# Kernel tuning notes

Hardware: AMD Instinct MI355X
Metric: run time of the kernel (lower is better)

Reference implementation:

```python
import jax, jax.numpy as jnp
import numpy as np

N, M, K, R, D = 2048, 64, 2, 512, 1024   # seq len, chunk size, neighbours, neighbour len, model dim
H, L = 16, 1024                           # heads, layer_size
LCH = N // M                              # number of chunks l = 32
DH = L // H
SCALE = 1.0 / (D ** 0.5)                  # source scales by input dim, not head dim


def setup_inputs() -> dict:
    key = jax.random.key(0)
    ks = jax.random.split(key, 6)
    s = 0.02
    return {
        "x": jax.random.normal(ks[0], (N, D), jnp.float32),
        "neighbours": jax.random.normal(ks[1], (LCH, K, R, D), jnp.float32),
        "Wq": jax.random.normal(ks[2], (L, D), jnp.float32) * s,
        "Wk": jax.random.normal(ks[3], (L, D), jnp.float32) * s,
        "Wv": jax.random.normal(ks[4], (L, D), jnp.float32) * s,
        "Wo": jax.random.normal(ks[5], (D, L), jnp.float32) * s,
    }


def _attend(q_in, ctx, Wq, Wk, Wv, Wo):
    # q_in: (B, Q, D) queries; ctx: (B, K, R, D) retrieved neighbours.
    # Batches the per-chunk, per-neighbour Attention calls of the source in one pass,
    # then means over the K neighbour axis (reduce 'k m d -> m d', 'mean').
    B, Q = q_in.shape[0], q_in.shape[1]
    q = (q_in @ Wq.T).reshape(B, Q, H, DH)                     # (B,Q,H,DH)
    kk = (ctx @ Wk.T).reshape(B, K, R, H, DH)                  # (B,K,R,H,DH)
    vv = (ctx @ Wv.T).reshape(B, K, R, H, DH)
    scores = jnp.einsum('bqhe,bkrhe->bkhrq', q, kk) * SCALE    # (B,K,H,R,Q)
    # FAITHFUL quirk: source softmaxes over the QUERY axis (last dim of 'b k q')
    w = jax.nn.softmax(scores, axis=-1)
    o = jnp.einsum('bkhrq,bkrhe->bkqhe', w, vv).reshape(B, K, Q, L)
    z = jnp.einsum('bkql,dl->bkqd', o, Wo)                     # output projection (dropout=0)
    return z.mean(axis=1)                                      # mean over neighbours -> (B,Q,D)


def reference(x, neighbours, Wq, Wk, Wv, Wo):
    # attending_chunks: shift input left by m-1, zero-pad bottom, chunk into (l, m, d)
    att = jnp.concatenate([x[M - 1:], jnp.zeros((M - 1, D), x.dtype)], axis=0).reshape(LCH, M, D)
    # main loop over chunks u in [0, l-2] and their k neighbours, fully batched
    main = _attend(att[:LCH - 1], neighbours[:LCH - 1], Wq, Wk, Wv, Wo)   # (l-1, M, D)
    # last token attends to neighbours[-1]
    last = _attend(x[-1][None, None, :], neighbours[-1][None], Wq, Wk, Wv, Wo)  # (1,1,D)
    body = jnp.concatenate([main.reshape(-1, D), att[-1]], axis=0)        # (N, D)
    # pad top with m-1 zeros, keep first n rows
    out = jnp.concatenate([jnp.zeros((M - 1, D), x.dtype), body[:N - M + 1]], axis=0)
    out = out.at[:M - 1].set(x[:M - 1])
    out = out.at[-1].set(last[0, 0])
    return out
```

## Files before the change

kernel.cpp:

```cpp
#include <hip/hip_runtime.h>
#include <hip/hip_bf16.h>


using u16 = unsigned short;
using u32 = unsigned int;

typedef float  f32x4   __attribute__((ext_vector_type(4)));
typedef __bf16 bf16x8v __attribute__((ext_vector_type(8)));
typedef __bf16 bf16x4v __attribute__((ext_vector_type(4)));
typedef short  s16x4   __attribute__((ext_vector_type(4)));
typedef u16    u16x8   __attribute__((ext_vector_type(8)));
typedef u16    u16x4v  __attribute__((ext_vector_type(4)));

#define SCALE_LOG2E (1.4426950408889634f / 32.0f)

__device__ __forceinline__ u16 f2b(float f){ return __builtin_bit_cast(u16, (__bf16)f); }
__device__ __forceinline__ int swz(int row, int cb){ return row*128 + (cb ^ ((row & 7) << 4)); }

__device__ __forceinline__ void gl_lds16(const void* g, void* l) {
    __builtin_amdgcn_global_load_lds(
        (const __attribute__((address_space(1))) unsigned int*)(unsigned long long)g,
        (__attribute__((address_space(3))) unsigned int*)(unsigned int)(unsigned long long)l,
        16, 0, 0);
}

__global__ __launch_bounds__(512, 2)
void gemm256(const u16* __restrict__ Ap, const u16* __restrict__ Bp,
             u16* __restrict__ Ka, u16* __restrict__ Vt,
             const u16* __restrict__ Aq, const u16* __restrict__ Bq,
             u16* __restrict__ Qa,
             int nKV, int nNt)
{
    __shared__ char Ls[131072];
    char* const Abase = Ls;
    char* const Bbase = Ls + 65536;

    const int tid  = threadIdx.x;
    const int lane = tid & 63, wave = tid >> 6;
    const int li = lane & 15, lg = lane >> 4;
    const int wr = wave >> 2, wc = wave & 3;

    const int nwg  = gridDim.x;
    const int lin  = blockIdx.x;
    const int lin2 = (lin & 7) * (nwg >> 3) + (lin >> 3);

    const bool isQ = (lin2 >= nKV);
    long bm, bn;
    if (isQ) { const int idx = lin2 - nKV; bm = (long)(idx >> 2) * 256; bn = (long)(idx & 3) * 256; }
    else     {                              bm = (long)(lin2 / nNt) * 256; bn = (long)(lin2 % nNt) * 256; }
    const u16* const Ag = isQ ? Aq : Ap;
    const u16* const Bg = isQ ? Bq : Bp;

    const int srow = tid >> 3;
    const int scol = ((tid & 7) ^ (srow & 7)) << 3;

    const u16* const pA0 = Ag + (bm + srow)*1024L + scol;
    const u16* const pA1 = Ag + (bm + 128 + srow)*1024L + scol;
    const u16* const pB0 = Bg + (bn + srow)*1024L + scol;
    const u16* const pB1 = Bg + (bn + 128 + srow)*1024L + scol;
    const long l64 = 64*1024L;

    auto stA = [&](int t, int hh) {
        char* d = Abase + (t & 1)*32768 + hh*16384 + wave*1024;
        const u16* p = (hh ? pA1 : pA0) + (long)t*64;
        gl_lds16(p, d);
        gl_lds16(p + l64, d + 8192);
    };
    auto stB = [&](int t, int hh) {
        char* d = Bbase + (t & 1)*32768 + hh*16384 + wave*1024;
        const u16* p = (hh ? pB1 : pB0) + (long)t*64;
        gl_lds16(p, d);
        gl_lds16(p + l64, d + 8192);
    };

    const int NT = 16;

    stB(0, 0); stB(0, 1); stA(0, 0); stA(0, 1); stB(1, 0);
    asm volatile("s_waitcnt vmcnt(2)" ::: "memory");
    asm volatile("s_barrier" ::: "memory");

    const int swx = (li & 7) << 4;
    const int cb0 = (lg*16) ^ swx;
    const int cb1 = (64 + lg*16) ^ swx;
    const int brb = (wc & 1)*64 + li;

    f32x4 acc[8][4] = {};
    bf16x8v av[4], aw[4], bv[4];

#define MFMA16(MH, AA, BB)                                                      \
    __builtin_amdgcn_s_setprio(1);                                              \
    _Pragma("unroll") for (int mt = 0; mt < 4; mt++)                            \
        _Pragma("unroll") for (int nt = 0; nt < 4; nt++)                        \
            acc[(MH)*4 + mt][nt] = __builtin_amdgcn_mfma_f32_16x16x32_bf16(     \
                (AA)[mt], (BB)[nt], acc[(MH)*4 + mt][nt], 0, 0, 0);             \
    __builtin_amdgcn_s_setprio(0);
#define RDA(DST, OFS, CB)                                                       \
    _Pragma("unroll") for (int i = 0; i < 4; i++)                               \
        (DST)[i] = *(const bf16x8v*)(At + (li + (OFS) + i*16)*128 + (CB));
#define RDB(DST, CB)                                                            \
    _Pragma("unroll") for (int i = 0; i < 4; i++)                               \
        (DST)[i] = *(const bf16x8v*)(Bt + (brb + i*16)*128 + (CB));

    for (int t = 0; t < NT; ++t) {
        char* At = Abase + (t & 1)*32768 + wr*16384;
        char* Bt = Bbase + (t & 1)*32768 + (wc >> 1)*16384;
        const bool s1 = (t + 1 < NT), s2 = (t + 2 < NT);

        RDA(av, 0, cb0); RDB(bv, cb0);
        if (s1) { stB(t + 1, 1); stA(t + 1, 0); }
        RDA(aw, 64, cb0);
        __builtin_amdgcn_sched_barrier(0);
        MFMA16(0, av, bv);
        if (s1) stA(t + 1, 1);
        RDA(av, 0, cb1);
        __builtin_amdgcn_sched_barrier(0);
        MFMA16(1, aw, bv);
        RDB(bv, cb1); RDA(aw, 64, cb1);
        __builtin_amdgcn_sched_barrier(0);
        MFMA16(0, av, bv);
        asm volatile("s_barrier" ::: "memory");
        if (s2) stB(t + 2, 0);
        MFMA16(1, aw, bv);
        if      (s2) { asm volatile("s_waitcnt vmcnt(2)" ::: "memory"); }
        else if (s1) { asm volatile("s_waitcnt vmcnt(0)" ::: "memory"); }
        asm volatile("s_barrier" ::: "memory");
    }
#undef MFMA16
#undef RDA
#undef RDB

    if (!isQ && bn >= 1024) {
        #pragma unroll
        for (int ai = 0; ai < 8; ai++) {
            const int m0 = wr*128 + (ai >> 2)*64 + (ai & 3)*16 + lg*4;
            #pragma unroll
            for (int nt = 0; nt < 4; nt++) {
                const int n = wc*64 + nt*16 + li;
                f32x4 c = acc[ai][nt];
                bf16x4v w;
                #pragma unroll
                for (int j = 0; j < 4; j++) w[j] = (__bf16)c[j];
                *(bf16x4v*)(Ls + n*512 + ((m0*2) ^ ((n & 31) << 4))) = w;
            }
        }
        __syncthreads();
        const int n    = tid >> 1;
        const int half = (tid & 1) * 128;
        u16* dst = Vt + (bn - 1024 + n)*32768L + bm + half;
        #pragma unroll
        for (int i = 0; i < 16; i++) {
            const int mb = (half + i*8) * 2;
            uint4 v = *(const uint4*)(Ls + n*512 + (mb ^ ((n & 31) << 4)));
            *(uint4*)(dst + i*8) = v;
        }
    } else {
        u16* Co = isQ ? Qa : Ka;
        #pragma unroll
        for (int ai = 0; ai < 8; ai++) {
            #pragma unroll
            for (int nt = 0; nt < 4; nt++) {
                f32x4 c = acc[ai][nt];
                const long row0 = bm + wr*128 + (ai >> 2)*64 + (ai & 3)*16 + lg*4;
                const long col  = bn + wc*64 + nt*16 + li;
                #pragma unroll
                for (int j = 0; j < 4; j++)
                    Co[(row0 + j)*1024 + col] = f2b(c[j]);
            }
        }
    }
}

template<bool AF32, int OM>
__global__ __launch_bounds__(256)
void gemm128(const void* __restrict__ Ap, int lda,
             const u16* __restrict__ Bp, int ldb,
             void* __restrict__ Cp, void* __restrict__ Cp2,
             int M, int Kc, int row_off, int nNt)
{
    __shared__ char As[128*128];
    __shared__ char Bs[128*128];
    const int tid  = threadIdx.x;
    const int lane = tid & 63, wave = tid >> 6;
    const int li = lane & 15, lg = lane >> 4;
    const int wr = wave >> 1, wc = wave & 1;

    const int nwg  = gridDim.x;
    const int lin  = blockIdx.x;
    const int lin2 = (lin & 7) * (nwg >> 3) + (lin >> 3);
    const long bm = (long)(lin2 / nNt) * 128;
    const long bn = (long)(lin2 % nNt) * 128;

    const int grow = wave*32 + (lane >> 3);
    const int gcol = ((lane & 7) ^ (lane >> 3)) << 3;
    const int sr = tid >> 1, sc = (tid & 1) * 32;
    long arow_f = bm + sr; if (arow_f >= M) arow_f = M - 1;
    long arow_g[4];
    #pragma unroll
    for (int j = 0; j < 4; j++) {
        long r = bm + grow + j*8;
        arow_g[j] = (r < M) ? r : (M - 1);
    }

    f32x4 acc[4][4] = {};

    for (int k0 = 0; k0 < Kc; k0 += 64) {
        float4 a4[8];
        if (AF32) {
            const float4* ap = (const float4*)((const float*)Ap + arow_f*lda + k0 + sc);
            #pragma unroll
            for (int i = 0; i < 8; i++) a4[i] = ap[i];
        }
        __syncthreads();
        if (!AF32) {
            #pragma unroll
            for (int j = 0; j < 4; j++)
                gl_lds16((const u16*)Ap + arow_g[j]*(long)lda + k0 + gcol,
                         As + (wave*4 + j)*1024);
        }
        #pragma unroll
        for (int j = 0; j < 4; j++)
            gl_lds16(Bp + (bn + grow + j*8)*(long)ldb + k0 + gcol,
                     Bs + (wave*4 + j)*1024);
        if (AF32) {
            #pragma unroll
            for (int i = 0; i < 4; i++) {
                float4 f0 = a4[2*i], f1 = a4[2*i+1];
                bf16x8v w;
                w[0]=(__bf16)f0.x; w[1]=(__bf16)f0.y; w[2]=(__bf16)f0.z; w[3]=(__bf16)f0.w;
                w[4]=(__bf16)f1.x; w[5]=(__bf16)f1.y; w[6]=(__bf16)f1.z; w[7]=(__bf16)f1.w;
                *(bf16x8v*)(As + swz(sr, sc*2 + i*16)) = w;
            }
        }
        __syncthreads();
        #pragma unroll
        for (int es = 0; es < 2; es++) {
            bf16x8v af[4], bfv[4];
            #pragma unroll
            for (int mt = 0; mt < 4; mt++)
                af[mt] = *(const bf16x8v*)(As + swz(wr*64 + mt*16 + li, es*64 + lg*16));
            #pragma unroll
            for (int nt = 0; nt < 4; nt++)
                bfv[nt] = *(const bf16x8v*)(Bs + swz(wc*64 + nt*16 + li, es*64 + lg*16));
            #pragma unroll
            for (int mt = 0; mt < 4; mt++)
                #pragma unroll
                for (int nt = 0; nt < 4; nt++)
                    acc[mt][nt] = __builtin_amdgcn_mfma_f32_16x16x32_bf16(
                        af[mt], bfv[nt], acc[mt][nt], 0, 0, 0);
        }
    }

    #pragma unroll
    for (int mt = 0; mt < 4; mt++) {
        #pragma unroll
        for (int nt = 0; nt < 4; nt++) {
            f32x4 c = acc[mt][nt];
            const long row0 = bm + wr*64 + mt*16 + lg*4;
            const long col  = bn + wc*64 + nt*16 + li;
            if (OM == 0) {
                u16* C = (u16*)Cp;
                #pragma unroll
                for (int j = 0; j < 4; j++) {
                    long rg = row0 + j;
                    if (rg < M) C[rg*1024 + col] = f2b(c[j]);
                }
            } else if (OM == 2) {
                float* C = (float*)Cp;
                #pragma unroll
                for (int j = 0; j < 4; j++) {
                    long rg = row0 + j;
                    if (rg < M) C[(row_off + rg)*1024 + col] = c[j];
                }
            } else {
                if (col < 1024) {
                    u16* Ka = (u16*)Cp;
                    #pragma unroll
                    for (int j = 0; j < 4; j++) Ka[(row0 + j)*1024 + col] = f2b(c[j]);
                } else {
                    u16* Vt = (u16*)Cp2;
                    bf16x4v w;
                    #pragma unroll
                    for (int j = 0; j < 4; j++) w[j] = (__bf16)c[j];
                    *(bf16x4v*)(Vt + (col - 1024)*32768L + row0) = w;
                }
            }
        }
    }
}

__global__ __launch_bounds__(256)
void attn_kernel(const u16* __restrict__ Qa, const u16* __restrict__ Ka,
                 const u16* __restrict__ Vt, u16* __restrict__ Om,
                 const float* __restrict__ x, float* __restrict__ out)
{
    const int u = blockIdx.x, h = blockIdx.y;
    const int tid = threadIdx.x;
    const int lane = tid & 63, wave = tid >> 6;
    const int li = lane & 15, lg = lane >> 4;

    if (u == 31) {
        #pragma unroll 4
        for (int it = 0; it < 16; ++it) {
            const int row = h*64 + it*4 + wave;
            const u16* p = Vt + (long)row*32768 + 31*1024 + lane*16;
            float s = 0.f;
            #pragma unroll
            for (int hf = 0; hf < 2; hf++) {
                bf16x8v v = *(const bf16x8v*)(p + hf*8);
                #pragma unroll
                for (int i = 0; i < 8; i++) s += (float)v[i];
            }
            #pragma unroll
            for (int m = 1; m < 64; m <<= 1) s += __shfl_xor(s, m);
            if (lane == 0) Om[(long)1984*1024 + row] = f2b(0.5f * s);
        }
        for (int i = h*1008 + tid; i < (h + 1)*1008; i += 256)
            ((float4*)out)[i] = ((const float4*)x)[i];
        return;
    }

    bf16x8v qf[4][2];
    #pragma unroll
    for (int qt = 0; qt < 4; qt++)
        #pragma unroll
        for (int es = 0; es < 2; es++)
            qf[qt][es] = *(const bf16x8v*)(Qa + (long)(63 + u*64 + qt*16 + li)*1024
                                              + h*64 + es*32 + lg*8);

    f32x4 acc[4][4] = {};

    for (int it = wave; it < 64; it += 4) {
        const int k = it >> 5, rsub = it & 31;
        const long kr = (long)u*1024 + k*512 + rsub*16;

        bf16x8v a0 = *(const bf16x8v*)(Ka + (kr + li)*1024 + h*64 + lg*8);
        bf16x8v a1 = *(const bf16x8v*)(Ka + (kr + li)*1024 + h*64 + 32 + lg*8);
        s16x4 va[4];
        #pragma unroll
        for (int et = 0; et < 4; et++)
            va[et] = *(const s16x4*)(Vt + (long)(h*64 + et*16 + li)*32768 + kr + lg*4);

        f32x4 s[4];
        #pragma unroll
        for (int qt = 0; qt < 4; qt++) {
            f32x4 c = {};
            c = __builtin_amdgcn_mfma_f32_16x16x32_bf16(a0, qf[qt][0], c, 0, 0, 0);
            c = __builtin_amdgcn_mfma_f32_16x16x32_bf16(a1, qf[qt][1], c, 0, 0, 0);
            s[qt] = c;
        }
        float p[4][4];
        #pragma unroll
        for (int qt = 0; qt < 4; qt++)
            #pragma unroll
            for (int j = 0; j < 4; j++)
                p[qt][j] = __builtin_amdgcn_exp2f(s[qt][j]);
        float rz[4];
        #pragma unroll
        for (int j = 0; j < 4; j++) {
            float z = p[0][j] + p[1][j] + p[2][j] + p[3][j];
            z += __shfl_xor(z, 1); z += __shfl_xor(z, 2);
            z += __shfl_xor(z, 4); z += __shfl_xor(z, 8);
            rz[j] = __builtin_amdgcn_rcpf(z);
        }
        s16x4 wf[4];
        #pragma unroll
        for (int qt = 0; qt < 4; qt++) {
            bf16x4v w;
            #pragma unroll
            for (int j = 0; j < 4; j++) w[j] = (__bf16)(p[qt][j] * rz[j]);
            wf[qt] = __builtin_bit_cast(s16x4, w);
        }
        #pragma unroll
        for (int et = 0; et < 4; et++)
            #pragma unroll
            for (int qt = 0; qt < 4; qt++)
                acc[et][qt] = __builtin_amdgcn_mfma_f32_16x16x16bf16_1k(
                    va[et], wf[qt], acc[et][qt], 0, 0, 0);
    }

    __shared__ float Osum[64*64];
    for (int w = 0; w < 4; w++) {
        if (wave == w) {
            #pragma unroll
            for (int et = 0; et < 4; et++)
                #pragma unroll
                for (int qt = 0; qt < 4; qt++)
                    #pragma unroll
                    for (int j = 0; j < 4; j++) {
                        int e = et*16 + lg*4 + j, q = qt*16 + li;
                        if (w == 0) Osum[e*64 + q]  = acc[et][qt][j];
                        else        Osum[e*64 + q] += acc[et][qt][j];
                    }
        }
        __syncthreads();
    }
    const int q = tid & 63, e0 = (tid >> 6) * 16;
    u16x8 o0, o1;
    #pragma unroll
    for (int i = 0; i < 8; i++) {
        o0[i] = f2b(0.5f * Osum[(e0 + i    )*64 + q]);
        o1[i] = f2b(0.5f * Osum[(e0 + 8 + i)*64 + q]);
    }
    u16* dst = Om + (long)(u*64 + q)*1024 + h*64 + e0;
    *(u16x8*)dst       = o0;
    *(u16x8*)(dst + 8) = o1;
}

__global__ __launch_bounds__(256)
void convert_all(const float* __restrict__ Wq, const float* __restrict__ Wk,
                 const float* __restrict__ Wv, const float* __restrict__ Wo,
                 const float* __restrict__ nb, const float* __restrict__ x,
                 u16* __restrict__ wW, u16* __restrict__ Anb,
                 u16* __restrict__ xb, int doA)
{
    const int NW = 524288, NN = 4194304, NX = 262144;
    const int tot = doA ? (NW + NN + NX) : NW;
    const int stride = gridDim.x*256;
    for (int i = blockIdx.x*256 + threadIdx.x; i < tot; i += stride) {
        const float* s; u16* d; float sc = 1.0f;
        if (i < NW) {
            int w = i >> 17;
            long off = (long)(i & 131071) * 8;
            s = (w == 0) ? Wq : (w == 1) ? Wk : (w == 2) ? Wv : Wo;
            s += off;
            d = wW + (long)w*1048576 + off;
            if (w == 0) sc = SCALE_LOG2E;
        } else if (i < NW + NN) {
            long off = (long)(i - NW) * 8;
            s = nb + off; d = Anb + off;
        } else {
            long off = (long)(i - NW - NN) * 8;
            s = x + off; d = xb + off;
        }
        float4 f0 = ((const float4*)s)[0], f1 = ((const float4*)s)[1];
        u16x8 o = { f2b(f0.x*sc), f2b(f0.y*sc), f2b(f0.z*sc), f2b(f0.w*sc),
                    f2b(f1.x*sc), f2b(f1.y*sc), f2b(f1.z*sc), f2b(f1.w*sc) };
        *(u16x8*)d = o;
    }
}

__global__ __launch_bounds__(256)
void tail_kernel(const u16* __restrict__ Vt, u16* __restrict__ Om,
                 const float* __restrict__ x, float* __restrict__ out)
{
    if (blockIdx.x < 256) {
        const int row  = blockIdx.x*4 + (threadIdx.x >> 6);
        const int lane = threadIdx.x & 63;
        const u16* p = Vt + (long)row*32768 + 31*1024 + lane*16;
        float s = 0.f;
        #pragma unroll
        for (int hf = 0; hf < 2; hf++) {
            bf16x8v v = *(const bf16x8v*)(p + hf*8);
            #pragma unroll
            for (int i = 0; i < 8; i++) s += (float)v[i];
        }
        #pragma unroll
        for (int m = 1; m < 64; m <<= 1) s += __shfl_xor(s, m);
        if (lane == 0) Om[(long)1984*1024 + row] = f2b(0.5f * s);
    } else {
        int i = (blockIdx.x - 256)*256 + threadIdx.x;
        ((float4*)out)[i] = ((const float4*)x)[i];
    }
}

extern "C" void kernel_launch(void* const* d_in, const int* in_sizes, int n_in,
                              void* d_out, int out_size, void* d_ws, size_t ws_size,
                              hipStream_t stream)
{
    const float* x  = (const float*)d_in[0];
    const float* nb = (const float*)d_in[1];
    const float* Wq = (const float*)d_in[2];
    const float* Wk = (const float*)d_in[3];
    const float* Wv = (const float*)d_in[4];
    const float* Wo = (const float*)d_in[5];
    float* out = (float*)d_out;
    char*  ws  = (char*)d_ws;

    if (ws_size < (size_t)144*1024*1024) return;
    const bool big = ws_size >= (size_t)212*1024*1024;
    u16* wW  = (u16*)ws;
    u16* Qa  = (u16*)(ws + (size_t) 8*1024*1024);
    u16* Om  = (u16*)(ws + (size_t)12*1024*1024);
    u16* Ka  = (u16*)(ws + (size_t)16*1024*1024);
    u16* Vt  = (u16*)(ws + (size_t)80*1024*1024);
    u16* Anb = (u16*)(ws + (size_t)144*1024*1024);
    u16* xb  = (u16*)(ws + (size_t)208*1024*1024);
    u16* wWq = wW, *wWk = wW + 1048576, *wWo = wW + 3*1048576;

    convert_all<<<dim3(4096), dim3(256), 0, stream>>>(
        Wq, Wk, Wv, Wo, nb, x, wW, Anb, xb, big ? 1 : 0);

    if (big) {
        gemm256<<<dim3(1056), dim3(512), 0, stream>>>(
            Anb, wWk, Ka, Vt, xb, wWq, Qa, 1024, 8);
        attn_kernel<<<dim3(32, 16), dim3(256), 0, stream>>>(Qa, Ka, Vt, Om, x, out);
    } else {
        gemm128<true, 0><<<dim3(128), dim3(256), 0, stream>>>(
            x, 1024, wWq, 1024, Qa, nullptr, 2048, 1024, 0, 8);
        gemm128<true, 3><<<dim3(4096), dim3(256), 0, stream>>>(
            nb, 1024, wWk, 1024, Ka, Vt, 32768, 1024, 0, 16);
        attn_kernel<<<dim3(32, 16), dim3(256), 0, stream>>>(Qa, Ka, Vt, Om, x, out);
    }

    gemm128<false, 2><<<dim3(128), dim3(256), 0, stream>>>(
        Om, 1024, wWo, 1024, out, nullptr, 1985, 1024, 63, 8);
}
```

Baseline: 244.1 us.

## Split-K the output projection GEMM across 256 blocks with a combine kernel

The Wo projection in the large-workspace path now splits the K dimension in two halves, launching 256 workgroups instead of 128 so more compute units are busy. Each half writes fp32 partials into reused workspace, and a new elementwise kernel sums them into the output rows. This adds extra global memory traffic for the partials and one more kernel launch in exchange for better GPU occupancy on a small GEMM.

```diff
diff --git a/kernel.cpp b/kernel.cpp
--- a/kernel.cpp
+++ b/kernel.cpp
@@ -186,9 +186,12 @@
 
     const int nwg  = gridDim.x;
     const int lin  = blockIdx.x;
-    const int lin2 = (lin & 7) * (nwg >> 3) + (lin >> 3);
+    int lin2 = (lin & 7) * (nwg >> 3) + (lin >> 3);
+    int kh = 0;
+    if (OM == 5) { kh = lin2 >= 128; lin2 -= kh*128; }
     const long bm = (long)(lin2 / nNt) * 128;
     const long bn = (long)(lin2 % nNt) * 128;
+    const int kbase = (OM == 5) ? kh*512 : 0;
 
     const int grow = wave*32 + (lane >> 3);
     const int gcol = ((lane & 7) ^ (lane >> 3)) << 3;
@@ -203,7 +206,8 @@
 
     f32x4 acc[4][4] = {};
 
-    for (int k0 = 0; k0 < Kc; k0 += 64) {
+    for (int k0c = 0; k0c < Kc; k0c += 64) {
+        const int k0 = k0c + kbase;
         float4 a4[8];
         if (AF32) {
             const float4* ap = (const float4*)((const float*)Ap + arow_f*lda + k0 + sc);
@@ -270,6 +274,13 @@
                 for (int j = 0; j < 4; j++) {
                     long rg = row0 + j;
                     if (rg < M) C[(row_off + rg)*1024 + col] = c[j];
+                }
+            } else if (OM == 5) {
+                float* C = kh ? (float*)Cp2 : (float*)Cp;
+                #pragma unroll
+                for (int j = 0; j < 4; j++) {
+                    long rg = row0 + j;
+                    if (rg < M) C[rg*1024 + col] = c[j];
                 }
             } else {
                 if (col < 1024) {
@@ -286,6 +297,17 @@
             }
         }
     }
+}
+
+__global__ __launch_bounds__(256)
+void combine_wo(const float* __restrict__ Pa, const float* __restrict__ Pb,
+                float* __restrict__ out)
+{
+    const long i = ((long)blockIdx.x*256 + threadIdx.x) * 4;
+    f32x4 a = *(const f32x4*)(Pa + i);
+    f32x4 b = *(const f32x4*)(Pb + i);
+    f32x4 r = { a[0]+b[0], a[1]+b[1], a[2]+b[2], a[3]+b[3] };
+    *(f32x4*)(out + 63*1024 + i) = r;
 }
 
 __global__ __launch_bounds__(256)
@@ -439,30 +461,6 @@
     }
 }
 
-__global__ __launch_bounds__(256)
-void tail_kernel(const u16* __restrict__ Vt, u16* __restrict__ Om,
-                 const float* __restrict__ x, float* __restrict__ out)
-{
-    if (blockIdx.x < 256) {
-        const int row  = blockIdx.x*4 + (threadIdx.x >> 6);
-        const int lane = threadIdx.x & 63;
-        const u16* p = Vt + (long)row*32768 + 31*1024 + lane*16;
-        float s = 0.f;
-        #pragma unroll
-        for (int hf = 0; hf < 2; hf++) {
-            bf16x8v v = *(const bf16x8v*)(p + hf*8);
-            #pragma unroll
-            for (int i = 0; i < 8; i++) s += (float)v[i];
-        }
-        #pragma unroll
-        for (int m = 1; m < 64; m <<= 1) s += __shfl_xor(s, m);
-        if (lane == 0) Om[(long)1984*1024 + row] = f2b(0.5f * s);
-    } else {
-        int i = (blockIdx.x - 256)*256 + threadIdx.x;
-        ((float4*)out)[i] = ((const float4*)x)[i];
-    }
-}
-
 extern "C" void kernel_launch(void* const* d_in, const int* in_sizes, int n_in,
                               void* d_out, int out_size, void* d_ws, size_t ws_size,
                               hipStream_t stream)
@@ -485,6 +483,8 @@
     u16* Vt  = (u16*)(ws + (size_t)80*1024*1024);
     u16* Anb = (u16*)(ws + (size_t)144*1024*1024);
     u16* xb  = (u16*)(ws + (size_t)208*1024*1024);
+    float* Pa = (float*)(ws + (size_t)144*1024*1024);
+    float* Pb = (float*)(ws + (size_t)160*1024*1024);
     u16* wWq = wW, *wWk = wW + 1048576, *wWo = wW + 3*1048576;
 
     convert_all<<<dim3(4096), dim3(256), 0, stream>>>(
@@ -494,14 +494,16 @@
         gemm256<<<dim3(1056), dim3(512), 0, stream>>>(
             Anb, wWk, Ka, Vt, xb, wWq, Qa, 1024, 8);
         attn_kernel<<<dim3(32, 16), dim3(256), 0, stream>>>(Qa, Ka, Vt, Om, x, out);
+        gemm128<false, 5><<<dim3(256), dim3(256), 0, stream>>>(
+            Om, 1024, wWo, 1024, Pa, Pb, 1985, 512, 0, 8);
+        combine_wo<<<dim3(1985), dim3(256), 0, stream>>>(Pa, Pb, out);
     } else {
         gemm128<true, 0><<<dim3(128), dim3(256), 0, stream>>>(
             x, 1024, wWq, 1024, Qa, nullptr, 2048, 1024, 0, 8);
         gemm128<true, 3><<<dim3(4096), dim3(256), 0, stream>>>(
             nb, 1024, wWk, 1024, Ka, Vt, 32768, 1024, 0, 16);
         attn_kernel<<<dim3(32, 16), dim3(256), 0, stream>>>(Qa, Ka, Vt, Om, x, out);
-    }
-
-    gemm128<false, 2><<<dim3(128), dim3(256), 0, stream>>>(
-        Om, 1024, wWo, 1024, out, nullptr, 1985, 1024, 63, 8);
-}
+        gemm128<false, 2><<<dim3(128), dim3(256), 0, stream>>>(
+            Om, 1024, wWo, 1024, out, nullptr, 1985, 1024, 63, 8);
+    }
+}
```

Measured after the change: 241.3 us. About the same (-1.2%).
